# Optimization experiments

Hardware: AMD Instinct MI355X
Metric: run time of the kernel (lower is better)

The kernel has to match this reference:

```python
import jax, jax.numpy as jnp
import numpy as np

DIM = 4096
N_HEADS = 32
HEAD_DIM = 128
N_KV_HEADS = 8
KV_REPEATS = N_HEADS // N_KV_HEADS
SLIDING_WINDOW = 4096
SEQLEN = 2048
SCALE = HEAD_DIM ** -0.5
NEG = -1e9


def calculate_rope(x, cos, sin):
    # x: [S, H, D]; cos/sin: [S, D//2] applied to interleaved channel pairs
    x1, x2 = x[..., ::2], x[..., 1::2]
    c, s = cos[:, None, :], sin[:, None, :]
    r1 = x1 * c - x2 * s
    r2 = x1 * s + x2 * c
    return jnp.stack([r1, r2], axis=-1).reshape(x.shape)


def setup_inputs() -> dict:
    key = jax.random.key(0)
    ks = jax.random.split(key, 8)
    x = jax.random.normal(ks[0], (SEQLEN, DIM), dtype=jnp.float32)
    # rotary tables
    inv_freq = 1.0 / (10000.0 ** (np.arange(0, HEAD_DIM, 2, dtype=np.float32) / HEAD_DIM))
    t = np.arange(SEQLEN, dtype=np.float32)
    freqs = np.outer(t, inv_freq)  # [S, D/2]
    cos_freq = jnp.asarray(np.cos(freqs), dtype=jnp.float32)
    sin_freq = jnp.asarray(np.sin(freqs), dtype=jnp.float32)
    positions = jnp.arange(SEQLEN, dtype=jnp.int32)
    # causal sliding-window additive mask
    i = np.arange(SEQLEN)[:, None]
    j = np.arange(SEQLEN)[None, :]
    allow = (j <= i) & (j > i - SLIDING_WINDOW)
    mask = jnp.asarray(np.where(allow, 0.0, NEG), dtype=jnp.float32)
    cache_k = jnp.zeros((SLIDING_WINDOW, N_KV_HEADS, HEAD_DIM), dtype=jnp.float32)
    cache_v = jnp.zeros((SLIDING_WINDOW, N_KV_HEADS, HEAD_DIM), dtype=jnp.float32)
    # eqx.nn.Linear weights have shape (out_features, in_features)
    sd = DIM ** -0.5
    wq = jax.random.normal(ks[1], (N_HEADS * HEAD_DIM, DIM), dtype=jnp.float32) * sd
    wk = jax.random.normal(ks[2], (N_KV_HEADS * HEAD_DIM, DIM), dtype=jnp.float32) * sd
    wv = jax.random.normal(ks[3], (N_KV_HEADS * HEAD_DIM, DIM), dtype=jnp.float32) * sd
    wo = jax.random.normal(ks[4], (DIM, N_HEADS * HEAD_DIM), dtype=jnp.float32) * (N_HEADS * HEAD_DIM) ** -0.5
    return {"x": x, "cos_freq": cos_freq, "sin_freq": sin_freq, "positions": positions,
            "mask": mask, "cache_k": cache_k, "cache_v": cache_v,
            "wq": wq, "wk": wk, "wv": wv, "wo": wo}


def reference(x, cos_freq, sin_freq, positions, mask, cache_k, cache_v, wq, wk, wv, wo):
    seqlen = x.shape[0]
    xq = (x @ wq.T).reshape(seqlen, N_HEADS, HEAD_DIM)
    xk = (x @ wk.T).reshape(seqlen, N_KV_HEADS, HEAD_DIM)
    xv = (x @ wv.T).reshape(seqlen, N_KV_HEADS, HEAD_DIM)
    xq = calculate_rope(xq, cos_freq, sin_freq)
    xk = calculate_rope(xk, cos_freq, sin_freq)
    # prefill branch (positions.shape[0] > 1): scatter into sliding-window cache
    cache_k = cache_k.at[positions, :, :].set(xk[positions, :, :], mode='drop')
    cache_v = cache_v.at[positions, :, :].set(xv[positions, :, :], mode='drop')
    # GQA repeat kv heads
    k = jnp.repeat(xk, KV_REPEATS, axis=1)  # [S, H, D]
    v = jnp.repeat(xv, KV_REPEATS, axis=1)
    # scores: [H, Sq, Sk]
    scores = jnp.einsum('qhd,khd->hqk', xq, k) * SCALE
    scores = scores + mask[None, ...]
    probs = jax.nn.softmax(scores.astype(jnp.float32), axis=-1).astype(xq.dtype)
    out = jnp.einsum('hqk,khd->qhd', probs, v).reshape(seqlen, N_HEADS * HEAD_DIM)
    output = out @ wo.T
    return output, cache_k, cache_v
```

## Files before the change

kernel.cpp:

```cpp
#include <hip/hip_runtime.h>

typedef unsigned short ushort_t;
typedef unsigned int uint_t;
typedef __attribute__((ext_vector_type(8))) short bf16x8;
typedef __attribute__((ext_vector_type(4))) float floatx4;

#define SEQ 2048
#define DIM 4096
#define NH 32
#define NKV 8
#define HD 128
#define KVDIM 1024
#define QKVN 6144

__device__ __forceinline__ ushort_t f2b(float f) {
  union { float f; uint_t u; } x; x.f = f;
  uint_t u = x.u;
  u += 0x7fffu + ((u >> 16) & 1u);
  return (ushort_t)(u >> 16);
}

#define GLOAD_LDS(g, l) \
  __builtin_amdgcn_global_load_lds((const __attribute__((address_space(1))) void*)(g), \
                                   (__attribute__((address_space(3))) void*)(l), 16, 0, 0)

__global__ __launch_bounds__(256) void cvt_bf16(const float* __restrict__ src,
                                                ushort_t* __restrict__ dst, int n8) {
  int i = blockIdx.x * 256 + threadIdx.x;
  if (i >= n8) return;
  const float4* s = (const float4*)src;
  float4 a = s[2 * i], b = s[2 * i + 1];
  union { ushort_t u[8]; uint4 v; } o;
  o.u[0] = f2b(a.x); o.u[1] = f2b(a.y); o.u[2] = f2b(a.z); o.u[3] = f2b(a.w);
  o.u[4] = f2b(b.x); o.u[5] = f2b(b.y); o.u[6] = f2b(b.z); o.u[7] = f2b(b.w);
  ((uint4*)dst)[i] = o.v;
}

__global__ __launch_bounds__(256) void gemm128(const ushort_t* __restrict__ A,
                                               const ushort_t* __restrict__ B,
                                               float* __restrict__ C,
                                               int N, int K) {
  __shared__ __attribute__((aligned(16))) ushort_t lds_a[128 * 32];
  __shared__ __attribute__((aligned(16))) ushort_t lds_b[128 * 32];
  int tid = threadIdx.x;
  int lane = tid & 63;
  int w = tid >> 6;
  int m0 = blockIdx.y * 128, n0 = blockIdx.x * 128;
  int wm = (w >> 1) * 64, wn = (w & 1) * 64;
  int row = lane & 15, quad = lane >> 4;

  int sr = tid >> 2;
  int sc = (tid & 3) * 8;
  const ushort_t* Ag = A + (size_t)(m0 + sr) * K + sc;
  const ushort_t* Bg = B + (size_t)(n0 + sr) * K + sc;
  ushort_t* la0 = &lds_a[(tid & ~63) * 8];
  ushort_t* lb0 = &lds_b[(tid & ~63) * 8];

  floatx4 acc[4][4] = {};
  for (int k0 = 0; k0 < K; k0 += 32) {
    GLOAD_LDS(Ag + k0, la0);
    GLOAD_LDS(Ag + (size_t)64 * K + k0, la0 + 2048);
    GLOAD_LDS(Bg + k0, lb0);
    GLOAD_LDS(Bg + (size_t)64 * K + k0, lb0 + 2048);
    __syncthreads();
    bf16x8 af[4], bfr[4];
#pragma unroll
    for (int i = 0; i < 4; ++i) af[i] = *(const bf16x8*)&lds_a[(wm + i * 16 + row) * 32 + quad * 8];
#pragma unroll
    for (int j = 0; j < 4; ++j) bfr[j] = *(const bf16x8*)&lds_b[(wn + j * 16 + row) * 32 + quad * 8];
#pragma unroll
    for (int i = 0; i < 4; ++i)
#pragma unroll
      for (int j = 0; j < 4; ++j)
        acc[i][j] = __builtin_amdgcn_mfma_f32_16x16x32_bf16(af[i], bfr[j], acc[i][j], 0, 0, 0);
    __syncthreads();
  }
#pragma unroll
  for (int i = 0; i < 4; ++i)
#pragma unroll
    for (int j = 0; j < 4; ++j) {
      float* Cp = C + (size_t)(m0 + wm + i * 16 + quad * 4) * N + n0 + wn + j * 16 + row;
#pragma unroll
      for (int r = 0; r < 4; ++r) Cp[(size_t)r * N] = acc[i][j][r];
    }
}

__global__ __launch_bounds__(256) void rope_q(const float* __restrict__ qkv,
                                              const float* __restrict__ cosf,
                                              const float* __restrict__ sinf,
                                              ushort_t* __restrict__ qb) {
  const float QS = 1.4426950408889634f * 0.08838834764831845f;
  int idx = blockIdx.x * 256 + threadIdx.x;
  int pos = idx >> 11;
  int p = idx & 2047;
  int h = p >> 6, i = p & 63;
  size_t sb = (size_t)pos * QKVN + h * HD + 2 * i;
  float x1 = qkv[sb], x2 = qkv[sb + 1];
  float c = cosf[pos * 64 + i], s = sinf[pos * 64 + i];
  float r1 = (x1 * c - x2 * s) * QS;
  float r2 = (x1 * s + x2 * c) * QS;
  size_t db = (size_t)pos * DIM + h * HD + 2 * i;
  ((uint_t*)qb)[db >> 1] = (uint_t)f2b(r1) | ((uint_t)f2b(r2) << 16);
}

__global__ __launch_bounds__(256) void rope_k(const float* __restrict__ qkv,
                                              const float* __restrict__ cosf,
                                              const float* __restrict__ sinf,
                                              ushort_t* __restrict__ kb,
                                              float* __restrict__ cache_k) {
  int idx = blockIdx.x * 256 + threadIdx.x;
  int pos = idx >> 9;
  int p = idx & 511;
  int kvh = p >> 6, i = p & 63;
  size_t sb = (size_t)pos * QKVN + DIM + kvh * HD + 2 * i;
  float x1 = qkv[sb], x2 = qkv[sb + 1];
  float c = cosf[pos * 64 + i], s = sinf[pos * 64 + i];
  float r1 = x1 * c - x2 * s;
  float r2 = x1 * s + x2 * c;
  size_t db = (size_t)pos * KVDIM + kvh * HD + 2 * i;
  ((uint_t*)kb)[db >> 1] = (uint_t)f2b(r1) | ((uint_t)f2b(r2) << 16);
  float2 cv; cv.x = r1; cv.y = r2;
  ((float2*)cache_k)[db >> 1] = cv;
}

__global__ __launch_bounds__(256) void vt_cache(const float* __restrict__ qkv,
                                                ushort_t* __restrict__ vtb,
                                                float* __restrict__ cache_v) {
  __shared__ float tile[64][65];
  int pos0 = blockIdx.x * 64, c0 = blockIdx.y * 64;
  int t = threadIdx.x;
  int pr = t >> 4, cq = (t & 15) * 4;
#pragma unroll
  for (int rr = 0; rr < 4; ++rr) {
    int prow = pr + rr * 16;
    float4 v = *(const float4*)(qkv + (size_t)(pos0 + prow) * QKVN + DIM + KVDIM + c0 + cq);
    *(float4*)(cache_v + (size_t)(pos0 + prow) * KVDIM + c0 + cq) = v;
    tile[prow][cq] = v.x; tile[prow][cq + 1] = v.y;
    tile[prow][cq + 2] = v.z; tile[prow][cq + 3] = v.w;
  }
  __syncthreads();
  int dc = t >> 2, pg = (t & 3) * 16;
  int kvh = c0 >> 7, dl = (c0 & 127) + dc;
  union { ushort_t u[16]; uint4 q[2]; } o;
#pragma unroll
  for (int e = 0; e < 16; ++e) o.u[e] = f2b(tile[pg + e][dc]);
  uint4* dst = (uint4*)(vtb + (size_t)kvh * (HD * SEQ) + (size_t)dl * SEQ + pos0 + pg);
  dst[0] = o.q[0]; dst[1] = o.q[1];
}

__global__ __launch_bounds__(256) void zero_tail(float* __restrict__ out) {
  int i = blockIdx.x * 256 + threadIdx.x;
  float4 z = {0.f, 0.f, 0.f, 0.f};
  ((float4*)(out + 10485760))[i] = z;
  ((float4*)(out + 14680064))[i] = z;
}

__global__ __launch_bounds__(256) void attn(const ushort_t* __restrict__ Q,
                                            const ushort_t* __restrict__ Kb,
                                            const ushort_t* __restrict__ Vt,
                                            ushort_t* __restrict__ O) {
  int h = blockIdx.y;
  int kvh = h >> 2;
  int tid = threadIdx.x;
  int w = tid >> 6, lane = tid & 63;
  int row = lane & 15, quad = lane >> 4;

  __shared__ __attribute__((aligned(16))) ushort_t lds_k[64][136];
  __shared__ __attribute__((aligned(16))) ushort_t lds_vt[128][72];
  __shared__ __attribute__((aligned(16))) float p_lds[4][16][68];

  int kr = tid >> 2, kc = (tid & 3) * 32;
  int vd = tid >> 1, vj = (tid & 1) * 32;
  const ushort_t* kg = Kb + (size_t)kr * KVDIM + kvh * HD + kc;
  const ushort_t* vg = Vt + (size_t)kvh * (HD * SEQ) + (size_t)vd * SEQ + vj;

#pragma unroll 1
  for (int ph = 0; ph < 2; ++ph) {
    int qb = ph ? (31 - blockIdx.x) : blockIdx.x;
    int q0 = qb * 64 + w * 16;

    bf16x8 qf[4];
    const ushort_t* qp = Q + (size_t)(q0 + row) * DIM + h * HD + quad * 8;
#pragma unroll
    for (int ks = 0; ks < 4; ++ks) qf[ks] = *(const bf16x8*)(qp + ks * 32);

    floatx4 o_acc[8] = {};
    float l_r[4] = {0.f, 0.f, 0.f, 0.f};

    for (int kt = 0; kt <= qb; ++kt) {
      int kv0 = kt * 64;
#pragma unroll
      for (int e = 0; e < 4; ++e)
        *(bf16x8*)&lds_k[kr][kc + e * 8] = *(const bf16x8*)(kg + (size_t)kv0 * KVDIM + e * 8);
#pragma unroll
      for (int e = 0; e < 4; ++e)
        *(bf16x8*)&lds_vt[vd][vj + e * 8] = *(const bf16x8*)(vg + kv0 + e * 8);
      __syncthreads();

      floatx4 s[4] = {};
#pragma unroll
      for (int j2 = 0; j2 < 4; ++j2)
#pragma unroll
        for (int ks = 0; ks < 4; ++ks) {
          bf16x8 kfrag = *(const bf16x8*)&lds_k[j2 * 16 + row][ks * 32 + quad * 8];
          s[j2] = __builtin_amdgcn_mfma_f32_16x16x32_bf16(qf[ks], kfrag, s[j2], 0, 0, 0);
        }

      bool diag = (kt == qb);
      float pv[4][4];
#pragma unroll
      for (int j2 = 0; j2 < 4; ++j2)
#pragma unroll
        for (int r = 0; r < 4; ++r) {
          float v = s[j2][r];
          if (diag) {
            int j_g = kv0 + j2 * 16 + row;
            int i_g = q0 + quad * 4 + r;
            v += (j_g <= i_g) ? 0.f : -1e9f;
          }
          float p = exp2f(v);
          pv[j2][r] = p;
          l_r[r] += p;
        }
#pragma unroll
      for (int j2 = 0; j2 < 4; ++j2)
#pragma unroll
        for (int r = 0; r < 4; ++r) p_lds[w][quad * 4 + r][j2 * 16 + row] = pv[j2][r];
      bf16x8 pf[2];
#pragma unroll
      for (int kb2 = 0; kb2 < 2; ++kb2) {
        float4 pa = *(const float4*)&p_lds[w][row][kb2 * 32 + quad * 8];
        float4 pb = *(const float4*)&p_lds[w][row][kb2 * 32 + quad * 8 + 4];
        union { bf16x8 v; ushort_t u[8]; } pu;
        pu.u[0] = f2b(pa.x); pu.u[1] = f2b(pa.y); pu.u[2] = f2b(pa.z); pu.u[3] = f2b(pa.w);
        pu.u[4] = f2b(pb.x); pu.u[5] = f2b(pb.y); pu.u[6] = f2b(pb.z); pu.u[7] = f2b(pb.w);
        pf[kb2] = pu.v;
      }
#pragma unroll
      for (int db = 0; db < 8; ++db)
#pragma unroll
        for (int kb2 = 0; kb2 < 2; ++kb2) {
          bf16x8 vfrag = *(const bf16x8*)&lds_vt[db * 16 + row][kb2 * 32 + quad * 8];
          o_acc[db] = __builtin_amdgcn_mfma_f32_16x16x32_bf16(pf[kb2], vfrag, o_acc[db], 0, 0, 0);
        }
      __syncthreads();
    }

#pragma unroll
    for (int off = 1; off < 16; off <<= 1)
#pragma unroll
      for (int r = 0; r < 4; ++r) l_r[r] += __shfl_xor(l_r[r], off, 64);
    float inv[4];
#pragma unroll
    for (int r = 0; r < 4; ++r) inv[r] = 1.0f / l_r[r];
#pragma unroll
    for (int db = 0; db < 8; ++db)
#pragma unroll
      for (int r = 0; r < 4; ++r)
        O[(size_t)(q0 + quad * 4 + r) * DIM + h * HD + db * 16 + row] = f2b(o_acc[db][r] * inv[r]);
  }
}

extern "C" void kernel_launch(void* const* d_in, const int* in_sizes, int n_in,
                              void* d_out, int out_size, void* d_ws, size_t ws_size,
                              hipStream_t stream) {
  const float* x    = (const float*)d_in[0];
  const float* cosf = (const float*)d_in[1];
  const float* sinf = (const float*)d_in[2];
  const float* wq = (const float*)d_in[7];
  const float* wk = (const float*)d_in[8];
  const float* wv = (const float*)d_in[9];
  const float* wo = (const float*)d_in[10];
  float* out = (float*)d_out;
  float* cache_k_out = out + 8388608;
  float* cache_v_out = out + 12582912;

  char* ws = (char*)d_ws;
  ushort_t* xb     = (ushort_t*)(ws + 0);
  ushort_t* wqkvb  = (ushort_t*)(ws + 16777216);
  ushort_t* wob    = (ushort_t*)(ws + 67108864);
  float*    qkv32  = (float*)(ws + 100663296);
  ushort_t* qbuf   = (ushort_t*)(ws + 150994944);
  ushort_t* kbuf   = (ushort_t*)(ws + 167772160);
  ushort_t* vtb    = (ushort_t*)(ws + 171966464);
  ushort_t* attnb  = (ushort_t*)(ws + 176160768);

  cvt_bf16<<<4096, 256, 0, stream>>>(x, xb, 1048576);
  cvt_bf16<<<8192, 256, 0, stream>>>(wq, wqkvb, 2097152);
  cvt_bf16<<<2048, 256, 0, stream>>>(wk, wqkvb + 16777216, 524288);
  cvt_bf16<<<2048, 256, 0, stream>>>(wv, wqkvb + 20971520, 524288);
  cvt_bf16<<<8192, 256, 0, stream>>>(wo, wob, 2097152);
  gemm128<<<dim3(48, 16), 256, 0, stream>>>(xb, wqkvb, qkv32, QKVN, DIM);
  rope_q<<<16384, 256, 0, stream>>>(qkv32, cosf, sinf, qbuf);
  rope_k<<<4096, 256, 0, stream>>>(qkv32, cosf, sinf, kbuf, cache_k_out);
  vt_cache<<<dim3(32, 16), 256, 0, stream>>>(qkv32, vtb, cache_v_out);
  zero_tail<<<2048, 256, 0, stream>>>(out);
  attn<<<dim3(16, 32), 256, 0, stream>>>(qbuf, kbuf, vtb, attnb);
  gemm128<<<dim3(32, 16), 256, 0, stream>>>(attnb, wob, out, DIM, DIM);
}
```

Baseline: 622.0 us.

## Use 32x32x16 MFMA with BK=64 swizzled LDS in GEMM and merge small kernels

The GEMM now stages 64-wide K tiles into LDS with an XOR swizzle and computes with 32x32x16 bf16 MFMA, holding a 2x2 grid of 32x32 accumulators per wave. This halves the number of loop iterations and barriers and aims to reduce LDS bank conflicts. Separately, the five conversion launches are merged into one kernel, and rope_q, rope_k and zero_tail are merged into one kernel, to cut launch overhead. LDS use per block doubles, which may lower occupancy.

```diff
diff --git a/kernel.cpp b/kernel.cpp
--- a/kernel.cpp
+++ b/kernel.cpp
@@ -4,6 +4,7 @@
 typedef unsigned int uint_t;
 typedef __attribute__((ext_vector_type(8))) short bf16x8;
 typedef __attribute__((ext_vector_type(4))) float floatx4;
+typedef __attribute__((ext_vector_type(16))) float floatx16;
 
 #define SEQ 2048
 #define DIM 4096
@@ -24,15 +25,26 @@
   __builtin_amdgcn_global_load_lds((const __attribute__((address_space(1))) void*)(g), \
                                    (__attribute__((address_space(3))) void*)(l), 16, 0, 0)
 
-__global__ __launch_bounds__(256) void cvt_bf16(const float* __restrict__ src,
-                                                ushort_t* __restrict__ dst, int n8) {
-  int i = blockIdx.x * 256 + threadIdx.x;
-  if (i >= n8) return;
+__global__ __launch_bounds__(256) void cvt_all(const float* __restrict__ x,
+                                               const float* __restrict__ wq,
+                                               const float* __restrict__ wk,
+                                               const float* __restrict__ wv,
+                                               const float* __restrict__ wo,
+                                               ushort_t* __restrict__ xb,
+                                               ushort_t* __restrict__ wqkvb,
+                                               ushort_t* __restrict__ wob) {
+  int b = blockIdx.x;
+  const float* src; ushort_t* dst; int i;
+  if (b < 4096)       { src = x;  dst = xb;               i = b * 256 + threadIdx.x; }
+  else if (b < 12288) { src = wq; dst = wqkvb;            i = (b - 4096) * 256 + threadIdx.x; }
+  else if (b < 14336) { src = wk; dst = wqkvb + 16777216; i = (b - 12288) * 256 + threadIdx.x; }
+  else if (b < 16384) { src = wv; dst = wqkvb + 20971520; i = (b - 14336) * 256 + threadIdx.x; }
+  else                { src = wo; dst = wob;              i = (b - 16384) * 256 + threadIdx.x; }
   const float4* s = (const float4*)src;
-  float4 a = s[2 * i], b = s[2 * i + 1];
+  float4 a = s[2 * i], c = s[2 * i + 1];
   union { ushort_t u[8]; uint4 v; } o;
   o.u[0] = f2b(a.x); o.u[1] = f2b(a.y); o.u[2] = f2b(a.z); o.u[3] = f2b(a.w);
-  o.u[4] = f2b(b.x); o.u[5] = f2b(b.y); o.u[6] = f2b(b.z); o.u[7] = f2b(b.w);
+  o.u[4] = f2b(c.x); o.u[5] = f2b(c.y); o.u[6] = f2b(c.z); o.u[7] = f2b(c.w);
   ((uint4*)dst)[i] = o.v;
 }
 
@@ -40,87 +52,108 @@
                                                const ushort_t* __restrict__ B,
                                                float* __restrict__ C,
                                                int N, int K) {
-  __shared__ __attribute__((aligned(16))) ushort_t lds_a[128 * 32];
-  __shared__ __attribute__((aligned(16))) ushort_t lds_b[128 * 32];
+  __shared__ __attribute__((aligned(16))) ushort_t lds_a[128 * 64];
+  __shared__ __attribute__((aligned(16))) ushort_t lds_b[128 * 64];
   int tid = threadIdx.x;
   int lane = tid & 63;
   int w = tid >> 6;
   int m0 = blockIdx.y * 128, n0 = blockIdx.x * 128;
   int wm = (w >> 1) * 64, wn = (w & 1) * 64;
-  int row = lane & 15, quad = lane >> 4;
-
-  int sr = tid >> 2;
-  int sc = (tid & 3) * 8;
-  const ushort_t* Ag = A + (size_t)(m0 + sr) * K + sc;
-  const ushort_t* Bg = B + (size_t)(n0 + sr) * K + sc;
-  ushort_t* la0 = &lds_a[(tid & ~63) * 8];
-  ushort_t* lb0 = &lds_b[(tid & ~63) * 8];
-
-  floatx4 acc[4][4] = {};
-  for (int k0 = 0; k0 < K; k0 += 32) {
-    GLOAD_LDS(Ag + k0, la0);
-    GLOAD_LDS(Ag + (size_t)64 * K + k0, la0 + 2048);
-    GLOAD_LDS(Bg + k0, lb0);
-    GLOAD_LDS(Bg + (size_t)64 * K + k0, lb0 + 2048);
+  int r32 = lane & 31, half = lane >> 5;
+
+  const ushort_t* Ag[4]; const ushort_t* Bg[4];
+  ushort_t* la[4]; ushort_t* lb[4];
+#pragma unroll
+  for (int e = 0; e < 4; ++e) {
+    int l = e * 256 + tid;
+    int row = l >> 3;
+    int cg = (l & 7) ^ (row & 7);
+    Ag[e] = A + (size_t)(m0 + row) * K + cg * 8;
+    Bg[e] = B + (size_t)(n0 + row) * K + cg * 8;
+    la[e] = &lds_a[(size_t)(e * 256 + (tid & ~63)) * 8];
+    lb[e] = &lds_b[(size_t)(e * 256 + (tid & ~63)) * 8];
+  }
+
+  floatx16 acc[2][2] = {};
+  for (int k0 = 0; k0 < K; k0 += 64) {
+#pragma unroll
+    for (int e = 0; e < 4; ++e) GLOAD_LDS(Ag[e] + k0, la[e]);
+#pragma unroll
+    for (int e = 0; e < 4; ++e) GLOAD_LDS(Bg[e] + k0, lb[e]);
     __syncthreads();
-    bf16x8 af[4], bfr[4];
-#pragma unroll
-    for (int i = 0; i < 4; ++i) af[i] = *(const bf16x8*)&lds_a[(wm + i * 16 + row) * 32 + quad * 8];
-#pragma unroll
-    for (int j = 0; j < 4; ++j) bfr[j] = *(const bf16x8*)&lds_b[(wn + j * 16 + row) * 32 + quad * 8];
-#pragma unroll
-    for (int i = 0; i < 4; ++i)
-#pragma unroll
-      for (int j = 0; j < 4; ++j)
-        acc[i][j] = __builtin_amdgcn_mfma_f32_16x16x32_bf16(af[i], bfr[j], acc[i][j], 0, 0, 0);
+#pragma unroll
+    for (int ks = 0; ks < 4; ++ks) {
+      int c = ks * 2 + half;
+      bf16x8 af[2], bfr[2];
+#pragma unroll
+      for (int mt = 0; mt < 2; ++mt) {
+        int row = wm + mt * 32 + r32;
+        af[mt] = *(const bf16x8*)&lds_a[row * 64 + (c ^ (row & 7)) * 8];
+      }
+#pragma unroll
+      for (int nt = 0; nt < 2; ++nt) {
+        int row = wn + nt * 32 + r32;
+        bfr[nt] = *(const bf16x8*)&lds_b[row * 64 + (c ^ (row & 7)) * 8];
+      }
+#pragma unroll
+      for (int mt = 0; mt < 2; ++mt)
+#pragma unroll
+        for (int nt = 0; nt < 2; ++nt)
+          acc[mt][nt] = __builtin_amdgcn_mfma_f32_32x32x16_bf16(af[mt], bfr[nt], acc[mt][nt], 0, 0, 0);
+    }
     __syncthreads();
   }
 #pragma unroll
-  for (int i = 0; i < 4; ++i)
-#pragma unroll
-    for (int j = 0; j < 4; ++j) {
-      float* Cp = C + (size_t)(m0 + wm + i * 16 + quad * 4) * N + n0 + wn + j * 16 + row;
-#pragma unroll
-      for (int r = 0; r < 4; ++r) Cp[(size_t)r * N] = acc[i][j][r];
-    }
-}
-
-__global__ __launch_bounds__(256) void rope_q(const float* __restrict__ qkv,
-                                              const float* __restrict__ cosf,
-                                              const float* __restrict__ sinf,
-                                              ushort_t* __restrict__ qb) {
-  const float QS = 1.4426950408889634f * 0.08838834764831845f;
-  int idx = blockIdx.x * 256 + threadIdx.x;
-  int pos = idx >> 11;
-  int p = idx & 2047;
-  int h = p >> 6, i = p & 63;
-  size_t sb = (size_t)pos * QKVN + h * HD + 2 * i;
-  float x1 = qkv[sb], x2 = qkv[sb + 1];
-  float c = cosf[pos * 64 + i], s = sinf[pos * 64 + i];
-  float r1 = (x1 * c - x2 * s) * QS;
-  float r2 = (x1 * s + x2 * c) * QS;
-  size_t db = (size_t)pos * DIM + h * HD + 2 * i;
-  ((uint_t*)qb)[db >> 1] = (uint_t)f2b(r1) | ((uint_t)f2b(r2) << 16);
-}
-
-__global__ __launch_bounds__(256) void rope_k(const float* __restrict__ qkv,
-                                              const float* __restrict__ cosf,
-                                              const float* __restrict__ sinf,
-                                              ushort_t* __restrict__ kb,
-                                              float* __restrict__ cache_k) {
-  int idx = blockIdx.x * 256 + threadIdx.x;
-  int pos = idx >> 9;
-  int p = idx & 511;
-  int kvh = p >> 6, i = p & 63;
-  size_t sb = (size_t)pos * QKVN + DIM + kvh * HD + 2 * i;
-  float x1 = qkv[sb], x2 = qkv[sb + 1];
-  float c = cosf[pos * 64 + i], s = sinf[pos * 64 + i];
-  float r1 = x1 * c - x2 * s;
-  float r2 = x1 * s + x2 * c;
-  size_t db = (size_t)pos * KVDIM + kvh * HD + 2 * i;
-  ((uint_t*)kb)[db >> 1] = (uint_t)f2b(r1) | ((uint_t)f2b(r2) << 16);
-  float2 cv; cv.x = r1; cv.y = r2;
-  ((float2*)cache_k)[db >> 1] = cv;
+  for (int mt = 0; mt < 2; ++mt)
+#pragma unroll
+    for (int nt = 0; nt < 2; ++nt)
+#pragma unroll
+      for (int reg = 0; reg < 16; ++reg) {
+        int rrow = (reg & 3) + 8 * (reg >> 2) + 4 * half;
+        C[(size_t)(m0 + wm + mt * 32 + rrow) * N + n0 + wn + nt * 32 + r32] = acc[mt][nt][reg];
+      }
+}
+
+__global__ __launch_bounds__(256) void posteps(const float* __restrict__ qkv,
+                                               const float* __restrict__ cosf,
+                                               const float* __restrict__ sinf,
+                                               ushort_t* __restrict__ qb,
+                                               ushort_t* __restrict__ kb,
+                                               float* __restrict__ out) {
+  int b = blockIdx.x;
+  if (b < 16384) {
+    const float QS = 1.4426950408889634f * 0.08838834764831845f;
+    int idx = b * 256 + threadIdx.x;
+    int pos = idx >> 11;
+    int p = idx & 2047;
+    int h = p >> 6, i = p & 63;
+    size_t sb = (size_t)pos * QKVN + h * HD + 2 * i;
+    float x1 = qkv[sb], x2 = qkv[sb + 1];
+    float c = cosf[pos * 64 + i], s = sinf[pos * 64 + i];
+    float r1 = (x1 * c - x2 * s) * QS;
+    float r2 = (x1 * s + x2 * c) * QS;
+    size_t db = (size_t)pos * DIM + h * HD + 2 * i;
+    ((uint_t*)qb)[db >> 1] = (uint_t)f2b(r1) | ((uint_t)f2b(r2) << 16);
+  } else if (b < 20480) {
+    int idx = (b - 16384) * 256 + threadIdx.x;
+    int pos = idx >> 9;
+    int p = idx & 511;
+    int kvh = p >> 6, i = p & 63;
+    size_t sb = (size_t)pos * QKVN + DIM + kvh * HD + 2 * i;
+    float x1 = qkv[sb], x2 = qkv[sb + 1];
+    float c = cosf[pos * 64 + i], s = sinf[pos * 64 + i];
+    float r1 = x1 * c - x2 * s;
+    float r2 = x1 * s + x2 * c;
+    size_t db = (size_t)pos * KVDIM + kvh * HD + 2 * i;
+    ((uint_t*)kb)[db >> 1] = (uint_t)f2b(r1) | ((uint_t)f2b(r2) << 16);
+    float2 cv; cv.x = r1; cv.y = r2;
+    ((float2*)(out + 8388608))[db >> 1] = cv;
+  } else {
+    int i = (b - 20480) * 256 + threadIdx.x;
+    float4 z = {0.f, 0.f, 0.f, 0.f};
+    ((float4*)(out + 10485760))[i] = z;
+    ((float4*)(out + 14680064))[i] = z;
+  }
 }
 
 __global__ __launch_bounds__(256) void vt_cache(const float* __restrict__ qkv,
@@ -146,13 +179,6 @@
   for (int e = 0; e < 16; ++e) o.u[e] = f2b(tile[pg + e][dc]);
   uint4* dst = (uint4*)(vtb + (size_t)kvh * (HD * SEQ) + (size_t)dl * SEQ + pos0 + pg);
   dst[0] = o.q[0]; dst[1] = o.q[1];
-}
-
-__global__ __launch_bounds__(256) void zero_tail(float* __restrict__ out) {
-  int i = blockIdx.x * 256 + threadIdx.x;
-  float4 z = {0.f, 0.f, 0.f, 0.f};
-  ((float4*)(out + 10485760))[i] = z;
-  ((float4*)(out + 14680064))[i] = z;
 }
 
 __global__ __launch_bounds__(256) void attn(const ushort_t* __restrict__ Q,
@@ -272,7 +298,6 @@
   const float* wv = (const float*)d_in[9];
   const float* wo = (const float*)d_in[10];
   float* out = (float*)d_out;
-  float* cache_k_out = out + 8388608;
   float* cache_v_out = out + 12582912;
 
   char* ws = (char*)d_ws;
@@ -285,16 +310,10 @@
   ushort_t* vtb    = (ushort_t*)(ws + 171966464);
   ushort_t* attnb  = (ushort_t*)(ws + 176160768);
 
-  cvt_bf16<<<4096, 256, 0, stream>>>(x, xb, 1048576);
-  cvt_bf16<<<8192, 256, 0, stream>>>(wq, wqkvb, 2097152);
-  cvt_bf16<<<2048, 256, 0, stream>>>(wk, wqkvb + 16777216, 524288);
-  cvt_bf16<<<2048, 256, 0, stream>>>(wv, wqkvb + 20971520, 524288);
-  cvt_bf16<<<8192, 256, 0, stream>>>(wo, wob, 2097152);
+  cvt_all<<<24576, 256, 0, stream>>>(x, wq, wk, wv, wo, xb, wqkvb, wob);
   gemm128<<<dim3(48, 16), 256, 0, stream>>>(xb, wqkvb, qkv32, QKVN, DIM);
-  rope_q<<<16384, 256, 0, stream>>>(qkv32, cosf, sinf, qbuf);
-  rope_k<<<4096, 256, 0, stream>>>(qkv32, cosf, sinf, kbuf, cache_k_out);
+  posteps<<<22528, 256, 0, stream>>>(qkv32, cosf, sinf, qbuf, kbuf, out);
   vt_cache<<<dim3(32, 16), 256, 0, stream>>>(qkv32, vtb, cache_v_out);
-  zero_tail<<<2048, 256, 0, stream>>>(out);
   attn<<<dim3(16, 32), 256, 0, stream>>>(qbuf, kbuf, vtb, attnb);
   gemm128<<<dim3(32, 16), 256, 0, stream>>>(attnb, wob, out, DIM, DIM);
 }
```

Measured after the change: 564.0 us. -9.3%, faster.
